# Performance work log

Measured on AMD Instinct MI355X. Metric: run time of the kernel, lower is better.

## Reference

```python
import jax, jax.numpy as jnp
import numpy as np

N_HEADS = 16
ROPE_BASE = 10000.0
EPS = float(np.finfo(np.float32).eps)  # F.rms_norm default eps for fp32


def _rms_norm(x):
    # RMSNorm over last dim, no learned scale (modded-nanogpt `norm`)
    return x * jax.lax.rsqrt(jnp.mean(jnp.square(x), axis=-1, keepdims=True) + EPS)


def _rotary(x):
    # x: [B, T, H, D]; non-interleaved half-rotation as in the Rotary module
    B, T, H, D = x.shape
    inv_freq = (1.0 / ROPE_BASE) ** (jnp.arange(0, D, 2, dtype=jnp.float32) / D)  # [D/2]
    t = jnp.arange(T, dtype=jnp.float32)
    freqs = jnp.outer(t, inv_freq)  # [T, D/2]
    cos = jnp.cos(freqs)[None, :, None, :]
    sin = jnp.sin(freqs)[None, :, None, :]
    x1, x2 = jnp.split(x, 2, axis=3)
    y1 = x1 * cos + x2 * sin
    y2 = -x1 * sin + x2 * cos
    return jnp.concatenate((y1, y2), axis=3).astype(x.dtype)


def setup_inputs() -> dict:
    key = jax.random.key(0)
    k1, k2, k3, k4 = jax.random.split(key, 4)
    B, T, Hs = 1, 2048, 2048
    d_head = Hs // N_HEADS
    std = 0.5 * d_head ** (-0.5)
    bound = 3 ** 0.5 * std
    x = jax.random.normal(k1, (B, T, Hs), dtype=jnp.float32)
    Wqkv = jax.random.uniform(k2, (3, Hs, Hs), dtype=jnp.float32, minval=-bound, maxval=bound)
    Wo_w = jax.random.normal(k3, (Hs, Hs), dtype=jnp.float32) * (Hs ** -0.5)
    Wo_b = jax.random.normal(k4, (Hs,), dtype=jnp.float32) * 0.01
    return {"x": x, "Wqkv": Wqkv, "Wo_w": Wo_w, "Wo_b": Wo_b}


def reference(x, Wqkv, Wo_w, Wo_b):
    B, T, Hs = x.shape
    d_head = Hs // N_HEADS
    # fused QKV projection: F.linear(x, Wqkv.flatten(end_dim=1)) -> x @ W^T
    W = Wqkv.reshape(3 * Hs, Hs)
    qkv = jnp.einsum('bth,oh->bto', x, W).reshape(B, T, 3 * N_HEADS, d_head)
    q, k, v = jnp.split(qkv, 3, axis=-2)  # each [B, T, H, D]
    q, k = _rms_norm(q), _rms_norm(k)
    q, k = _rotary(q), _rotary(k)
    # causal attention (flex_attention block_mask = causal), scale = 1/sqrt(d)
    scale = 1.0 / jnp.sqrt(jnp.float32(d_head))
    scores = jnp.einsum('bthd,bshd->bhts', q, k) * scale  # [B, H, T, S]
    causal = jnp.tril(jnp.ones((T, T), dtype=bool))
    scores = jnp.where(causal[None, None], scores, jnp.float32(-1e30))
    probs = jax.nn.softmax(scores, axis=-1)
    y = jnp.einsum('bhts,bshd->bthd', probs, v).reshape(B, T, Hs)
    return jnp.einsum('bth,oh->bto', y, Wo_w) + Wo_b
```

## Files before the change

kernel.cpp:

```cpp
#include <hip/hip_runtime.h>
#include <hip/hip_bf16.h>
#include <stdint.h>

#define T_SEQ 2048
#define HS    2048
#define NH    16
#define DH    128
#define QKVN  (3*HS)

typedef __attribute__((ext_vector_type(8))) short          bf16x8;
typedef __attribute__((ext_vector_type(4))) float          f32x4;
typedef __attribute__((ext_vector_type(4))) unsigned short us4;
typedef __attribute__((ext_vector_type(8))) unsigned short us8;

__device__ __forceinline__ unsigned short f2bf(float x) {
  unsigned int u = __float_as_uint(x);
  return (unsigned short)((u + 0x7fffu + ((u >> 16) & 1u)) >> 16);
}

__device__ __forceinline__ void gl_lds16(const void* g, void* l) {
  __builtin_amdgcn_global_load_lds((__attribute__((address_space(1))) void*)g,
                                   (__attribute__((address_space(3))) void*)l, 16, 0, 0);
}

__global__ __launch_bounds__(256) void cast_bf16_kernel(const float* __restrict__ in,
                                                        unsigned short* __restrict__ out, int n) {
  int i = (blockIdx.x * 256 + threadIdx.x) * 8;
  if (i >= n) return;
  f32x4 a = *(const f32x4*)(in + i);
  f32x4 b = *(const f32x4*)(in + i + 4);
  us8 r;
#pragma unroll
  for (int j = 0; j < 4; ++j) { r[j] = f2bf(a[j]); r[j + 4] = f2bf(b[j]); }
  *(us8*)(out + i) = r;
}

__global__ __launch_bounds__(256) void rope_table_kernel(float* __restrict__ cosd,
                                                         float* __restrict__ sind) {
  int i = blockIdx.x * 256 + threadIdx.x;
  if (i >= T_SEQ * 64) return;
  int t = i >> 6, f = i & 63;
  float inv = expf(-9.210340371976184f * (float)f * (1.0f / 64.0f));
  float ang = (float)t * inv;
  float s, c;
  sincosf(ang, &s, &c);
  cosd[i] = c; sind[i] = s;
}

template <int BIAS>
__global__ __launch_bounds__(256, 2)
void gemm_bt(const unsigned short* __restrict__ A, const unsigned short* __restrict__ Bt,
             float* __restrict__ C, const float* __restrict__ bias, int M, int N, int K) {
  __shared__ unsigned short As[128 * 64];
  __shared__ unsigned short Bs[128 * 64];
  const int tid  = threadIdx.x;
  const int lane = tid & 63;
  const int w    = tid >> 6;
  const int fr   = lane & 15;
  const int fq   = lane >> 4;
  const int bm   = blockIdx.y * 128;
  const int bn   = blockIdx.x * 128;
  const int wr   = (w >> 1) * 64;
  const int wc   = (w & 1) * 64;

  f32x4 acc[4][4];
#pragma unroll
  for (int m = 0; m < 4; ++m)
#pragma unroll
    for (int n = 0; n < 4; ++n) { acc[m][n][0]=0.f; acc[m][n][1]=0.f; acc[m][n][2]=0.f; acc[m][n][3]=0.f; }

  const int srow = lane >> 3;
  const int scol = (lane & 7) * 8;
  const unsigned short* Ag = A + (long)bm * K;
  const unsigned short* Bg = Bt + (long)bn * K;

  const int nk = K >> 6;
  for (int kt = 0; kt < nk; ++kt) {
    const int k0 = kt << 6;
    __syncthreads();
#pragma unroll
    for (int i = 0; i < 4; ++i) {
      int r = i * 32 + w * 8;
      gl_lds16(Ag + (long)(r + srow) * K + k0 + scol, &As[r * 64]);
      gl_lds16(Bg + (long)(r + srow) * K + k0 + scol, &Bs[r * 64]);
    }
    __syncthreads();
#pragma unroll
    for (int ks = 0; ks < 2; ++ks) {
      bf16x8 af[4], bfr[4];
#pragma unroll
      for (int m = 0; m < 4; ++m) af[m]  = *(const bf16x8*)&As[(wr + m * 16 + fr) * 64 + ks * 32 + fq * 8];
#pragma unroll
      for (int n = 0; n < 4; ++n) bfr[n] = *(const bf16x8*)&Bs[(wc + n * 16 + fr) * 64 + ks * 32 + fq * 8];
#pragma unroll
      for (int m = 0; m < 4; ++m)
#pragma unroll
        for (int n = 0; n < 4; ++n)
          acc[m][n] = __builtin_amdgcn_mfma_f32_16x16x32_bf16(af[m], bfr[n], acc[m][n], 0, 0, 0);
    }
  }
#pragma unroll
  for (int m = 0; m < 4; ++m) {
    int row0 = bm + wr + m * 16 + fq * 4;
#pragma unroll
    for (int n = 0; n < 4; ++n) {
      int col = bn + wc + n * 16 + fr;
      float bv = BIAS ? bias[col] : 0.0f;
#pragma unroll
      for (int j = 0; j < 4; ++j)
        C[(long)(row0 + j) * N + col] = acc[m][n][j] + bv;
    }
  }
}

__global__ __launch_bounds__(128)
void normrope_qk(const float* __restrict__ qkv, const float* __restrict__ cosd,
                 const float* __restrict__ sind, unsigned short* __restrict__ qb,
                 unsigned short* __restrict__ kb) {
  const int t = blockIdx.x;
  const int y = blockIdx.y;
  const int kind = y >> 4;
  const int h = y & 15;
  const int d = threadIdx.x;
  float x = qkv[(long)t * QKVN + y * 128 + d];
  float ss = x * x;
#pragma unroll
  for (int m = 1; m < 64; m <<= 1) ss += __shfl_xor(ss, m, 64);
  __shared__ float red[2];
  __shared__ float xn[128];
  if ((d & 63) == 0) red[d >> 6] = ss;
  __syncthreads();
  ss = red[0] + red[1];
  float r = rsqrtf(ss * (1.0f / 128.0f) + 1.1920928955078125e-07f);
  float v = x * r;
  xn[d] = v;
  __syncthreads();
  float o;
  if (d < 64) {
    float c = cosd[t * 64 + d], s = sind[t * 64 + d];
    o = v * c + xn[d + 64] * s;
  } else {
    float c = cosd[t * 64 + d - 64], s = sind[t * 64 + d - 64];
    o = -xn[d - 64] * s + v * c;
  }
  unsigned short* dst = kind ? kb : qb;
  dst[((long)h * T_SEQ + t) * 128 + d] = f2bf(o);
}

__global__ __launch_bounds__(256)
void v_transpose(const float* __restrict__ qkv, unsigned short* __restrict__ vt) {
  const int tb = blockIdx.x;
  const int h  = blockIdx.y;
  __shared__ unsigned short vl[128][72];
  const int tid = threadIdx.x;
#pragma unroll
  for (int p = 0; p < 32; ++p) {
    int rr = p * 2 + (tid >> 7);
    int d  = tid & 127;
    float x = qkv[(long)(tb * 64 + rr) * QKVN + 2 * HS + h * 128 + d];
    vl[d][rr] = f2bf(x);
  }
  __syncthreads();
#pragma unroll
  for (int p = 0; p < 8; ++p) {
    int idx = (p * 256 + tid) * 4;
    int d = idx >> 6;
    int i = idx & 63;
    us4 val = *(const us4*)&vl[d][i];
    *(us4*)&vt[((long)h * DH + d) * T_SEQ + tb * 64 + i] = val;
  }
}

__global__ __launch_bounds__(256, 2)
void attn_kernel(const unsigned short* __restrict__ qg, const unsigned short* __restrict__ kg,
                 const unsigned short* __restrict__ vtg, unsigned short* __restrict__ yb) {
  const int bi = blockIdx.x;
  const int j  = (bi < 256) ? bi : bi - 256;
  const int h  = j & 15;
  const int q0 = j >> 4;
  const int qb = (bi < 256) ? (31 - q0) : q0;

  __shared__ unsigned short Ks[2][64 * 128];
  __shared__ unsigned short Vts[2][128 * 64];
  __shared__ unsigned short Ps[4][16 * 72];

  const int tid = threadIdx.x, lane = tid & 63, w = tid >> 6;
  const int fr = lane & 15, fq = lane >> 4;

  const unsigned short* qh = qg  + (long)h * T_SEQ * 128;
  const unsigned short* kh = kg  + (long)h * T_SEQ * 128;
  const unsigned short* vh = vtg + (long)h * 128 * T_SEQ;

  const int krow_off = lane >> 4;
  const int vrow_off = lane >> 3;
  const int vg       = (lane & 7) ^ vrow_off;

  {
#pragma unroll
    for (int i = 0; i < 4; ++i) {
      int c = w * 4 + i;
      int r = 4 * c + krow_off;
      int g = (lane & 15) ^ (r & 7);
      gl_lds16(kh + r * 128 + g * 8, &Ks[0][c * 512]);
    }
#pragma unroll
    for (int i = 0; i < 4; ++i) {
      int r0 = (w * 4 + i) * 8;
      gl_lds16(vh + (long)(r0 + vrow_off) * T_SEQ + vg * 8, &Vts[0][r0 * 64]);
    }
  }

  bf16x8 aq[4];
  {
    const unsigned short* qrow = qh + (long)(qb * 64 + w * 16 + fr) * 128;
#pragma unroll
    for (int ks = 0; ks < 4; ++ks)
      aq[ks] = *(const bf16x8*)(qrow + ks * 32 + fq * 8);
  }

  f32x4 acc[8];
#pragma unroll
  for (int n = 0; n < 8; ++n) { acc[n][0]=0.f; acc[n][1]=0.f; acc[n][2]=0.f; acc[n][3]=0.f; }
  float mrow[4], lrow[4];
#pragma unroll
  for (int j2 = 0; j2 < 4; ++j2) { mrow[j2] = -__builtin_huge_valf(); lrow[j2] = 0.f; }

  const float scale = 0.08838834764831845f;

  __syncthreads();

  for (int kt = 0; kt <= qb; ++kt) {
    const int cur = kt & 1;

    if (kt < qb) {
      const int nb = cur ^ 1;
      const unsigned short* ksrc = kh + (kt + 1) * (64 * 128);
      const unsigned short* vsrc = vh + (kt + 1) * 64;
#pragma unroll
      for (int i = 0; i < 4; ++i) {
        int c = w * 4 + i;
        int r = 4 * c + krow_off;
        int g = (lane & 15) ^ (r & 7);
        gl_lds16(ksrc + r * 128 + g * 8, &Ks[nb][c * 512]);
      }
#pragma unroll
      for (int i = 0; i < 4; ++i) {
        int r0 = (w * 4 + i) * 8;
        gl_lds16(vsrc + (long)(r0 + vrow_off) * T_SEQ + vg * 8, &Vts[nb][r0 * 64]);
      }
    }

    f32x4 sv[4];
#pragma unroll
    for (int n = 0; n < 4; ++n) { sv[n][0]=0.f; sv[n][1]=0.f; sv[n][2]=0.f; sv[n][3]=0.f; }
    __builtin_amdgcn_s_setprio(1);
#pragma unroll
    for (int ks = 0; ks < 4; ++ks)
#pragma unroll
      for (int n = 0; n < 4; ++n) {
        int R = n * 16 + fr;
        bf16x8 bk = *(const bf16x8*)&Ks[cur][R * 128 + (((ks * 4 + fq) ^ (fr & 7)) << 3)];
        sv[n] = __builtin_amdgcn_mfma_f32_16x16x32_bf16(aq[ks], bk, sv[n], 0, 0, 0);
      }
    __builtin_amdgcn_s_setprio(0);

#pragma unroll
    for (int n = 0; n < 4; ++n)
#pragma unroll
      for (int j3 = 0; j3 < 4; ++j3) {
        float s = sv[n][j3] * scale;
        if (kt == qb && (n * 16 + fr) > (w * 16 + fq * 4 + j3)) s = -__builtin_huge_valf();
        sv[n][j3] = s;
      }

    float pm[4];
#pragma unroll
    for (int j3 = 0; j3 < 4; ++j3)
      pm[j3] = fmaxf(fmaxf(sv[0][j3], sv[1][j3]), fmaxf(sv[2][j3], sv[3][j3]));
#pragma unroll
    for (int m = 1; m < 16; m <<= 1)
#pragma unroll
      for (int j3 = 0; j3 < 4; ++j3) pm[j3] = fmaxf(pm[j3], __shfl_xor(pm[j3], m, 64));

    float alpha[4];
#pragma unroll
    for (int j3 = 0; j3 < 4; ++j3) {
      float mn = fmaxf(mrow[j3], pm[j3]);
      alpha[j3] = __expf(mrow[j3] - mn);
      mrow[j3] = mn;
    }
    float rs[4] = {0.f, 0.f, 0.f, 0.f};
#pragma unroll
    for (int n = 0; n < 4; ++n)
#pragma unroll
      for (int j3 = 0; j3 < 4; ++j3) {
        float p = __expf(sv[n][j3] - mrow[j3]);
        sv[n][j3] = p;
        rs[j3] += p;
      }
#pragma unroll
    for (int m = 1; m < 16; m <<= 1)
#pragma unroll
      for (int j3 = 0; j3 < 4; ++j3) rs[j3] += __shfl_xor(rs[j3], m, 64);
#pragma unroll
    for (int j3 = 0; j3 < 4; ++j3) lrow[j3] = lrow[j3] * alpha[j3] + rs[j3];
#pragma unroll
    for (int n = 0; n < 8; ++n)
#pragma unroll
      for (int j3 = 0; j3 < 4; ++j3) acc[n][j3] *= alpha[j3];

    unsigned short* pl = &Ps[w][0];
#pragma unroll
    for (int n = 0; n < 4; ++n)
#pragma unroll
      for (int j3 = 0; j3 < 4; ++j3)
        pl[(fq * 4 + j3) * 72 + n * 16 + fr] = f2bf(sv[n][j3]);
    asm volatile("s_waitcnt lgkmcnt(0)" ::: "memory");
    __builtin_amdgcn_s_setprio(1);
#pragma unroll
    for (int ks = 0; ks < 2; ++ks) {
      bf16x8 pa = *(const bf16x8*)&pl[fr * 72 + ks * 32 + fq * 8];
#pragma unroll
      for (int n = 0; n < 8; ++n) {
        int R = n * 16 + fr;
        bf16x8 bv = *(const bf16x8*)&Vts[cur][R * 64 + (((ks * 4 + fq) ^ (fr & 7)) << 3)];
        acc[n] = __builtin_amdgcn_mfma_f32_16x16x32_bf16(pa, bv, acc[n], 0, 0, 0);
      }
    }
    __builtin_amdgcn_s_setprio(0);

    __syncthreads();
  }

#pragma unroll
  for (int j3 = 0; j3 < 4; ++j3) {
    float inv = 1.0f / lrow[j3];
    int t = qb * 64 + w * 16 + fq * 4 + j3;
#pragma unroll
    for (int n = 0; n < 8; ++n)
      yb[(long)t * HS + h * 128 + n * 16 + fr] = f2bf(acc[n][j3] * inv);
  }
}

extern "C" void kernel_launch(void* const* d_in, const int* in_sizes, int n_in,
                              void* d_out, int out_size, void* d_ws, size_t ws_size,
                              hipStream_t stream) {
  const float* x    = (const float*)d_in[0];
  const float* Wqkv = (const float*)d_in[1];
  const float* Wo_w = (const float*)d_in[2];
  const float* Wo_b = (const float*)d_in[3];
  float* out = (float*)d_out;
  char* ws = (char*)d_ws;

  unsigned short* xbf  = (unsigned short*)(ws + 0L);
  unsigned short* wqbf = (unsigned short*)(ws + 8388608L);
  unsigned short* wobf = (unsigned short*)(ws + 33554432L);
  float*          qkv  = (float*)         (ws + 41943040L);
  unsigned short* qb   = (unsigned short*)(ws + 92274688L);
  unsigned short* kb   = (unsigned short*)(ws + 100663296L);
  unsigned short* vt   = (unsigned short*)(ws + 109051904L);
  unsigned short* yb   = (unsigned short*)(ws + 117440512L);
  float*          cosd = (float*)         (ws + 125829120L);
  float*          sind = (float*)         (ws + 126353408L);

  cast_bf16_kernel<<<dim3(4194304 / 8 / 256), 256, 0, stream>>>(x, xbf, 4194304);
  cast_bf16_kernel<<<dim3(12582912 / 8 / 256), 256, 0, stream>>>(Wqkv, wqbf, 12582912);
  cast_bf16_kernel<<<dim3(4194304 / 8 / 256), 256, 0, stream>>>(Wo_w, wobf, 4194304);
  rope_table_kernel<<<dim3(512), 256, 0, stream>>>(cosd, sind);

  gemm_bt<0><<<dim3(QKVN / 128, T_SEQ / 128), 256, 0, stream>>>(xbf, wqbf, qkv, nullptr,
                                                                T_SEQ, QKVN, HS);
  normrope_qk<<<dim3(T_SEQ, 2 * NH), 128, 0, stream>>>(qkv, cosd, sind, qb, kb);
  v_transpose<<<dim3(T_SEQ / 64, NH), 256, 0, stream>>>(qkv, vt);
  attn_kernel<<<dim3(512), 256, 0, stream>>>(qb, kb, vt, yb);
  gemm_bt<1><<<dim3(HS / 128, T_SEQ / 128), 256, 0, stream>>>(yb, wobf, out, Wo_b,
                                                              T_SEQ, HS, HS);
}
```

Measured before the change: 322.8 us.

## Swizzle GEMM LDS, narrow output-projection tile, and restructure norm-rope kernel

The GEMM now XOR-swizzles LDS column groups to avoid bank conflicts on MFMA fragment reads. It raises s_setprio around the MFMA section and allows 4 blocks per CU. The output projection uses a 128x64 tile to launch more blocks and fill more CUs. The QK norm+rope kernel is rewritten to process one row per wavefront with float2 loads, a wave shuffle reduction and shuffle-based rotation instead of LDS and barriers. Risks include register pressure under the higher occupancy bound and lower reuse from the narrower tile.

```diff
diff --git a/kernel.cpp b/kernel.cpp
--- a/kernel.cpp
+++ b/kernel.cpp
@@ -47,30 +47,31 @@
   cosd[i] = c; sind[i] = s;
 }
 
-template <int BIAS>
-__global__ __launch_bounds__(256, 2)
+template <int BIAS, int BN>
+__global__ __launch_bounds__(256, 4)
 void gemm_bt(const unsigned short* __restrict__ A, const unsigned short* __restrict__ Bt,
              float* __restrict__ C, const float* __restrict__ bias, int M, int N, int K) {
+  constexpr int FN = BN / 32;
   __shared__ unsigned short As[128 * 64];
-  __shared__ unsigned short Bs[128 * 64];
+  __shared__ unsigned short Bs[BN * 64];
   const int tid  = threadIdx.x;
   const int lane = tid & 63;
   const int w    = tid >> 6;
   const int fr   = lane & 15;
   const int fq   = lane >> 4;
   const int bm   = blockIdx.y * 128;
-  const int bn   = blockIdx.x * 128;
+  const int bn   = blockIdx.x * BN;
   const int wr   = (w >> 1) * 64;
-  const int wc   = (w & 1) * 64;
-
-  f32x4 acc[4][4];
+  const int wc   = (w & 1) * (BN / 2);
+
+  f32x4 acc[4][FN];
 #pragma unroll
   for (int m = 0; m < 4; ++m)
 #pragma unroll
-    for (int n = 0; n < 4; ++n) { acc[m][n][0]=0.f; acc[m][n][1]=0.f; acc[m][n][2]=0.f; acc[m][n][3]=0.f; }
+    for (int n = 0; n < FN; ++n) { acc[m][n][0]=0.f; acc[m][n][1]=0.f; acc[m][n][2]=0.f; acc[m][n][3]=0.f; }
 
   const int srow = lane >> 3;
-  const int scol = (lane & 7) * 8;
+  const int sg   = (lane & 7) ^ srow;
   const unsigned short* Ag = A + (long)bm * K;
   const unsigned short* Bg = Bt + (long)bn * K;
 
@@ -81,29 +82,37 @@
 #pragma unroll
     for (int i = 0; i < 4; ++i) {
       int r = i * 32 + w * 8;
-      gl_lds16(Ag + (long)(r + srow) * K + k0 + scol, &As[r * 64]);
-      gl_lds16(Bg + (long)(r + srow) * K + k0 + scol, &Bs[r * 64]);
+      gl_lds16(Ag + (long)(r + srow) * K + k0 + sg * 8, &As[r * 64]);
+    }
+#pragma unroll
+    for (int i = 0; i < BN / 32; ++i) {
+      int r = i * 32 + w * 8;
+      gl_lds16(Bg + (long)(r + srow) * K + k0 + sg * 8, &Bs[r * 64]);
     }
     __syncthreads();
+    __builtin_amdgcn_s_setprio(1);
 #pragma unroll
     for (int ks = 0; ks < 2; ++ks) {
-      bf16x8 af[4], bfr[4];
-#pragma unroll
-      for (int m = 0; m < 4; ++m) af[m]  = *(const bf16x8*)&As[(wr + m * 16 + fr) * 64 + ks * 32 + fq * 8];
-#pragma unroll
-      for (int n = 0; n < 4; ++n) bfr[n] = *(const bf16x8*)&Bs[(wc + n * 16 + fr) * 64 + ks * 32 + fq * 8];
+      bf16x8 af[4], bfr[FN];
 #pragma unroll
       for (int m = 0; m < 4; ++m)
-#pragma unroll
-        for (int n = 0; n < 4; ++n)
+        af[m]  = *(const bf16x8*)&As[(wr + m * 16 + fr) * 64 + (((ks * 4 + fq) ^ (fr & 7)) << 3)];
+#pragma unroll
+      for (int n = 0; n < FN; ++n)
+        bfr[n] = *(const bf16x8*)&Bs[(wc + n * 16 + fr) * 64 + (((ks * 4 + fq) ^ (fr & 7)) << 3)];
+#pragma unroll
+      for (int m = 0; m < 4; ++m)
+#pragma unroll
+        for (int n = 0; n < FN; ++n)
           acc[m][n] = __builtin_amdgcn_mfma_f32_16x16x32_bf16(af[m], bfr[n], acc[m][n], 0, 0, 0);
     }
+    __builtin_amdgcn_s_setprio(0);
   }
 #pragma unroll
   for (int m = 0; m < 4; ++m) {
     int row0 = bm + wr + m * 16 + fq * 4;
 #pragma unroll
-    for (int n = 0; n < 4; ++n) {
+    for (int n = 0; n < FN; ++n) {
       int col = bn + wc + n * 16 + fr;
       float bv = BIAS ? bias[col] : 0.0f;
 #pragma unroll
@@ -113,38 +122,31 @@
   }
 }
 
-__global__ __launch_bounds__(128)
+__global__ __launch_bounds__(256)
 void normrope_qk(const float* __restrict__ qkv, const float* __restrict__ cosd,
                  const float* __restrict__ sind, unsigned short* __restrict__ qb,
                  unsigned short* __restrict__ kb) {
-  const int t = blockIdx.x;
-  const int y = blockIdx.y;
-  const int kind = y >> 4;
-  const int h = y & 15;
-  const int d = threadIdx.x;
-  float x = qkv[(long)t * QKVN + y * 128 + d];
-  float ss = x * x;
-#pragma unroll
-  for (int m = 1; m < 64; m <<= 1) ss += __shfl_xor(ss, m, 64);
-  __shared__ float red[2];
-  __shared__ float xn[128];
-  if ((d & 63) == 0) red[d >> 6] = ss;
-  __syncthreads();
-  ss = red[0] + red[1];
-  float r = rsqrtf(ss * (1.0f / 128.0f) + 1.1920928955078125e-07f);
-  float v = x * r;
-  xn[d] = v;
-  __syncthreads();
-  float o;
-  if (d < 64) {
-    float c = cosd[t * 64 + d], s = sind[t * 64 + d];
-    o = v * c + xn[d + 64] * s;
-  } else {
-    float c = cosd[t * 64 + d - 64], s = sind[t * 64 + d - 64];
-    o = -xn[d - 64] * s + v * c;
-  }
-  unsigned short* dst = kind ? kb : qb;
-  dst[((long)h * T_SEQ + t) * 128 + d] = f2bf(o);
+  const int wgl  = (blockIdx.x * 256 + threadIdx.x) >> 6;
+  const int lane = threadIdx.x & 63;
+  for (int rr = wgl; rr < T_SEQ * 32; rr += 4096) {
+    const int t = rr >> 5;
+    const int y = rr & 31;
+    const float2 v = *(const float2*)(qkv + (long)t * QKVN + y * 128 + lane * 2);
+    float ss = v.x * v.x + v.y * v.y;
+#pragma unroll
+    for (int m = 1; m < 64; m <<= 1) ss += __shfl_xor(ss, m, 64);
+    const float r = rsqrtf(ss * (1.0f / 128.0f) + 1.1920928955078125e-07f);
+    const float a = v.x * r, b = v.y * r;
+    const float pa = __shfl_xor(a, 32, 64), pb = __shfl_xor(b, 32, 64);
+    const float2 c2 = *(const float2*)(cosd + t * 64 + (lane & 31) * 2);
+    const float2 s2 = *(const float2*)(sind + t * 64 + (lane & 31) * 2);
+    float o0, o1;
+    if (lane < 32) { o0 =  a * c2.x + pa * s2.x;  o1 =  b * c2.y + pb * s2.y; }
+    else           { o0 = -pa * s2.x + a * c2.x;  o1 = -pb * s2.y + b * c2.y; }
+    unsigned short* dst = (y >> 4) ? kb : qb;
+    const unsigned int packed = (unsigned int)f2bf(o0) | ((unsigned int)f2bf(o1) << 16);
+    *(unsigned int*)(dst + ((long)(y & 15) * T_SEQ + t) * 128 + lane * 2) = packed;
+  }
 }
 
 __global__ __launch_bounds__(256)
@@ -368,11 +370,11 @@
   cast_bf16_kernel<<<dim3(4194304 / 8 / 256), 256, 0, stream>>>(Wo_w, wobf, 4194304);
   rope_table_kernel<<<dim3(512), 256, 0, stream>>>(cosd, sind);
 
-  gemm_bt<0><<<dim3(QKVN / 128, T_SEQ / 128), 256, 0, stream>>>(xbf, wqbf, qkv, nullptr,
-                                                                T_SEQ, QKVN, HS);
-  normrope_qk<<<dim3(T_SEQ, 2 * NH), 128, 0, stream>>>(qkv, cosd, sind, qb, kb);
+  gemm_bt<0, 128><<<dim3(QKVN / 128, T_SEQ / 128), 256, 0, stream>>>(xbf, wqbf, qkv, nullptr,
+                                                                     T_SEQ, QKVN, HS);
+  normrope_qk<<<dim3(1024), 256, 0, stream>>>(qkv, cosd, sind, qb, kb);
   v_transpose<<<dim3(T_SEQ / 64, NH), 256, 0, stream>>>(qkv, vt);
   attn_kernel<<<dim3(512), 256, 0, stream>>>(qb, kb, vt, yb);
-  gemm_bt<1><<<dim3(HS / 128, T_SEQ / 128), 256, 0, stream>>>(yb, wobf, out, Wo_b,
-                                                              T_SEQ, HS, HS);
-}
+  gemm_bt<1, 64><<<dim3(HS / 64, T_SEQ / 128), 256, 0, stream>>>(yb, wobf, out, Wo_b,
+                                                                 T_SEQ, HS, HS);
+}
```

New measurement: 297.4 us. 1.09x faster.
